# Kernel tuning notes

Measured on AMD Instinct MI355X. Metric: run time of the kernel, lower is better.

## Reference

```python
import jax, jax.numpy as jnp
import numpy as np

B, S, D = 16, 4096, 1024
DIM_K, DIM_V, NUM_HEAD = 1024, 1024, 16


def setup_inputs() -> dict:
    key = jax.random.key(0)
    ks = jax.random.split(key, 7)
    s_in = 1.0 / np.sqrt(D)
    return {
        "x": jax.random.normal(ks[0], (B, S, D), dtype=jnp.float32),
        "Wq": jax.random.normal(ks[1], (D, DIM_K), dtype=jnp.float32) * s_in,
        "bq": jnp.zeros((DIM_K,), dtype=jnp.float32),
        "Wk": jax.random.normal(ks[2], (D, DIM_K), dtype=jnp.float32) * s_in,
        "bk": jnp.zeros((DIM_K,), dtype=jnp.float32),
        "Wv": jax.random.normal(ks[3], (D, DIM_V), dtype=jnp.float32) * s_in,
        "bv": jnp.zeros((DIM_V,), dtype=jnp.float32),
    }


def reference(x, Wq, bq, Wk, bk, Wv, bv):
    H = NUM_HEAD
    b, s, _ = x.shape
    Q = x @ Wq + bq                      # (B,S,dim_k)
    K = x @ Wk + bk                      # (B,S,dim_k)
    V = x @ Wv + bv                      # (B,S,dim_v)
    Q_ = Q.reshape(b, s, H, DIM_K // H)  # (B,S,H,dk)
    K_ = K.reshape(b, s, H, DIM_K // H)
    V_ = V.reshape(b, s, H, DIM_V // H)
    # NOTE: faithful to the source quirk — scores are across HEADS (H x H)
    # at each (batch, seq) position; no 1/sqrt(dim_k) scaling (unused in source).
    scores = jnp.einsum("bshd,bsgd->bshg", Q_, K_)   # (B,S,H,H)
    atten = jax.nn.softmax(scores, axis=-1)
    out = jnp.einsum("bshg,bsgd->bshd", atten, V_)    # (B,S,H,dv_head)
    return out.reshape(b, s, -1)                      # (B,S,dim_v)
```

## Files before the change

### kernel.cpp

```cpp
#include <hip/hip_runtime.h>
#include <stdint.h>

#define M_TOTAL 65536
#define DIM     1024
#define NQKV    3072
#define NHEAD   16
#define HDIM    64

typedef __attribute__((ext_vector_type(8))) _Float16 f16x8;
typedef __attribute__((ext_vector_type(4))) _Float16 f16x4;
typedef __attribute__((ext_vector_type(4))) float    f32x4;

__global__ __launch_bounds__(256) void cvt_x_kernel(const float* __restrict__ x,
                                                    _Float16* __restrict__ xh,
                                                    int n4) {
    int i = blockIdx.x * blockDim.x + threadIdx.x;
    int stride = gridDim.x * blockDim.x;
    const float4* x4 = (const float4*)x;
    f16x4* o4 = (f16x4*)xh;
    for (; i < n4; i += stride) {
        float4 v = x4[i];
        f16x4 o;
        o[0] = (_Float16)v.x; o[1] = (_Float16)v.y;
        o[2] = (_Float16)v.z; o[3] = (_Float16)v.w;
        o4[i] = o;
    }
}

__global__ void cvt_w_kernel(const float* __restrict__ Wq,
                             const float* __restrict__ Wk,
                             const float* __restrict__ Wv,
                             _Float16* __restrict__ Wt) {
    __shared__ float tile[32][33];
    int which = blockIdx.z;
    const float* W = (which == 0) ? Wq : (which == 1) ? Wk : Wv;
    int d0 = blockIdx.y * 32, n0 = blockIdx.x * 32;
    int tx = threadIdx.x, ty = threadIdx.y;
    tile[ty][tx] = W[(size_t)(d0 + ty) * DIM + n0 + tx];
    __syncthreads();
    Wt[(size_t)(which * DIM + n0 + ty) * DIM + d0 + tx] = (_Float16)tile[tx][ty];
}

__global__ __launch_bounds__(256) void bias_kernel(const float* __restrict__ bq,
                                                   const float* __restrict__ bk,
                                                   const float* __restrict__ bv,
                                                   float* __restrict__ bias) {
    int i = blockIdx.x * 256 + threadIdx.x;
    if (i < NQKV)
        bias[i] = (i < 1024) ? bq[i] : (i < 2048) ? bk[i - 1024] : bv[i - 2048];
}


#define LDSA(slot)  ((slot) << 15)
#define LDSB(slot)  (65536 + ((slot) << 15))

#define MFMA_Q(MIBASE, NIBASE)                                                  \
    __builtin_amdgcn_s_setprio(1);                                              \
    _Pragma("unroll") for (int mi = 0; mi < 4; ++mi)                            \
    _Pragma("unroll") for (int ni = 0; ni < 2; ++ni)                            \
    _Pragma("unroll") for (int ks = 0; ks < 2; ++ks)                            \
        acc[(MIBASE) + mi][(NIBASE) + ni] = __builtin_amdgcn_mfma_f32_16x16x32_f16( \
            a[mi][ks], b[(NIBASE) + ni][ks], acc[(MIBASE) + mi][(NIBASE) + ni], 0, 0, 0); \
    __builtin_amdgcn_s_setprio(0);

__global__ __launch_bounds__(512, 2) void qkv_gemm_kernel(const _Float16* __restrict__ Xh,
                                                          const _Float16* __restrict__ Wth,
                                                          const float* __restrict__ bias,
                                                          _Float16* __restrict__ Ch) {
    extern __shared__ char smem[];

    const int bid = blockIdx.x;
    const int swz = (bid & 7) * (3072 / 8) + (bid >> 3);
    const int tm  = swz / (NQKV / 256);
    const int tn  = swz % (NQKV / 256);
    const int brow = tm * 256;
    const int bcol = tn * 256;

    const int tid = threadIdx.x;
    const int w   = tid >> 6;
    const int l   = tid & 63;
    const int wm  = w >> 2;
    const int wn  = w & 3;

    const int lrow8 = l >> 3;
    const int lcol8 = (l & 7) ^ lrow8;
    const _Float16* pAsrc = Xh  + (size_t)(brow + w * 8 + lrow8) * DIM + lcol8 * 8;
    const _Float16* pBsrc = Wth + (size_t)(bcol + w * 8 + lrow8) * DIM + lcol8 * 8;

    auto stA = [&](int slot, int kt, int half) {
        const _Float16* s = pAsrc + ((size_t)half << 17) + ((size_t)kt << 6);
        char* d = smem + LDSA(slot) + (half << 14) + (w << 10);
        __builtin_amdgcn_global_load_lds((const __attribute__((address_space(1))) void*)s,
                                         (__attribute__((address_space(3))) void*)d, 16, 0, 0);
        __builtin_amdgcn_global_load_lds((const __attribute__((address_space(1))) void*)(s + (1 << 16)),
                                         (__attribute__((address_space(3))) void*)(d + 8192), 16, 0, 0);
    };
    auto stB = [&](int slot, int kt, int half) {
        const _Float16* s = pBsrc + ((size_t)half << 17) + ((size_t)kt << 6);
        char* d = smem + LDSB(slot) + (half << 14) + (w << 10);
        __builtin_amdgcn_global_load_lds((const __attribute__((address_space(1))) void*)s,
                                         (__attribute__((address_space(3))) void*)d, 16, 0, 0);
        __builtin_amdgcn_global_load_lds((const __attribute__((address_space(1))) void*)(s + (1 << 16)),
                                         (__attribute__((address_space(3))) void*)(d + 8192), 16, 0, 0);
    };

    const int aRowB = ((wm << 7) + (l & 15)) << 7;
    const int bRowB = 65536 + (((wn << 6) + (l & 15)) << 7);
    const int xk0 = (((l >> 4) ^ (l & 7)) << 4);
    const int xk1 = ((((l >> 4) + 4) ^ (l & 7)) << 4);
    auto LDA = [&](int slot, int mi, int ks) -> f16x8 {
        return *(const f16x8*)(smem + (slot << 15) + aRowB + (mi << 11) + (ks ? xk1 : xk0));
    };
    auto LDB = [&](int slot, int ni, int ks) -> f16x8 {
        return *(const f16x8*)(smem + (slot << 15) + bRowB + (ni << 11) + (ks ? xk1 : xk0));
    };

    f32x4 acc[8][4] = {};
    f16x8 a[4][2], b[4][2];

    stB(0, 0, 0); stB(0, 0, 1);
    stA(0, 0, 0); stA(0, 0, 1);
    stB(1, 1, 0); stB(1, 1, 1);
    asm volatile("s_waitcnt vmcnt(4)" ::: "memory");
    __builtin_amdgcn_s_barrier();
    __builtin_amdgcn_sched_barrier(0);

#pragma unroll 1
    for (int i = 0; i < 7; ++i) {
        const int u = 2 * i;
#pragma unroll
        for (int mi = 0; mi < 4; ++mi) { a[mi][0] = LDA(0, mi, 0); a[mi][1] = LDA(0, mi, 1); }
#pragma unroll
        for (int ni = 0; ni < 2; ++ni) { b[ni][0] = LDB(0, ni, 0); b[ni][1] = LDB(0, ni, 1); }
        stA(1, u + 1, 0);
        __builtin_amdgcn_s_barrier();
        MFMA_Q(0, 0)
        __builtin_amdgcn_s_barrier();
        b[2][0] = LDB(0, 2, 0); b[2][1] = LDB(0, 2, 1);
        b[3][0] = LDB(0, 3, 0); b[3][1] = LDB(0, 3, 1);
        stA(1, u + 1, 1);
        __builtin_amdgcn_s_barrier();
        MFMA_Q(0, 2)
        __builtin_amdgcn_s_barrier();
#pragma unroll
        for (int mi = 0; mi < 4; ++mi) { a[mi][0] = LDA(0, mi + 4, 0); a[mi][1] = LDA(0, mi + 4, 1); }
        stB(0, u + 2, 0);
        __builtin_amdgcn_s_barrier();
        MFMA_Q(4, 0)
        __builtin_amdgcn_s_barrier();
        stB(0, u + 2, 1);
        asm volatile("s_waitcnt vmcnt(4)" ::: "memory");
        __builtin_amdgcn_s_barrier();
        __builtin_amdgcn_sched_barrier(0);
        MFMA_Q(4, 2)
        __builtin_amdgcn_s_barrier();
#pragma unroll
        for (int mi = 0; mi < 4; ++mi) { a[mi][0] = LDA(1, mi, 0); a[mi][1] = LDA(1, mi, 1); }
#pragma unroll
        for (int ni = 0; ni < 2; ++ni) { b[ni][0] = LDB(1, ni, 0); b[ni][1] = LDB(1, ni, 1); }
        stA(0, u + 2, 0);
        __builtin_amdgcn_s_barrier();
        MFMA_Q(0, 0)
        __builtin_amdgcn_s_barrier();
        b[2][0] = LDB(1, 2, 0); b[2][1] = LDB(1, 2, 1);
        b[3][0] = LDB(1, 3, 0); b[3][1] = LDB(1, 3, 1);
        stA(0, u + 2, 1);
        __builtin_amdgcn_s_barrier();
        MFMA_Q(0, 2)
        __builtin_amdgcn_s_barrier();
#pragma unroll
        for (int mi = 0; mi < 4; ++mi) { a[mi][0] = LDA(1, mi + 4, 0); a[mi][1] = LDA(1, mi + 4, 1); }
        stB(1, u + 3, 0);
        __builtin_amdgcn_s_barrier();
        MFMA_Q(4, 0)
        __builtin_amdgcn_s_barrier();
        stB(1, u + 3, 1);
        asm volatile("s_waitcnt vmcnt(4)" ::: "memory");
        __builtin_amdgcn_s_barrier();
        __builtin_amdgcn_sched_barrier(0);
        MFMA_Q(4, 2)
        __builtin_amdgcn_s_barrier();
    }

    {
#pragma unroll
        for (int mi = 0; mi < 4; ++mi) { a[mi][0] = LDA(0, mi, 0); a[mi][1] = LDA(0, mi, 1); }
#pragma unroll
        for (int ni = 0; ni < 2; ++ni) { b[ni][0] = LDB(0, ni, 0); b[ni][1] = LDB(0, ni, 1); }
        stA(1, 15, 0);
        __builtin_amdgcn_s_barrier();
        MFMA_Q(0, 0)
        __builtin_amdgcn_s_barrier();
        b[2][0] = LDB(0, 2, 0); b[2][1] = LDB(0, 2, 1);
        b[3][0] = LDB(0, 3, 0); b[3][1] = LDB(0, 3, 1);
        stA(1, 15, 1);
        __builtin_amdgcn_s_barrier();
        MFMA_Q(0, 2)
        __builtin_amdgcn_s_barrier();
#pragma unroll
        for (int mi = 0; mi < 4; ++mi) { a[mi][0] = LDA(0, mi + 4, 0); a[mi][1] = LDA(0, mi + 4, 1); }
        __builtin_amdgcn_s_barrier();
        MFMA_Q(4, 0)
        __builtin_amdgcn_s_barrier();
        asm volatile("s_waitcnt vmcnt(0)" ::: "memory");
        __builtin_amdgcn_s_barrier();
        __builtin_amdgcn_sched_barrier(0);
        MFMA_Q(4, 2)
        __builtin_amdgcn_s_barrier();
#pragma unroll
        for (int mi = 0; mi < 4; ++mi) { a[mi][0] = LDA(1, mi, 0); a[mi][1] = LDA(1, mi, 1); }
#pragma unroll
        for (int ni = 0; ni < 2; ++ni) { b[ni][0] = LDB(1, ni, 0); b[ni][1] = LDB(1, ni, 1); }
        __builtin_amdgcn_s_barrier();
        MFMA_Q(0, 0)
        __builtin_amdgcn_s_barrier();
        b[2][0] = LDB(1, 2, 0); b[2][1] = LDB(1, 2, 1);
        b[3][0] = LDB(1, 3, 0); b[3][1] = LDB(1, 3, 1);
        __builtin_amdgcn_s_barrier();
        MFMA_Q(0, 2)
        __builtin_amdgcn_s_barrier();
#pragma unroll
        for (int mi = 0; mi < 4; ++mi) { a[mi][0] = LDA(1, mi + 4, 0); a[mi][1] = LDA(1, mi + 4, 1); }
        __builtin_amdgcn_s_barrier();
        MFMA_Q(4, 0)
        MFMA_Q(4, 2)
    }

    const int r4 = (l >> 4) << 2;
#pragma unroll
    for (int ni = 0; ni < 4; ++ni) {
        const int col = bcol + (wn << 6) + (ni << 4) + (l & 15);
        const float bv = bias[col];
#pragma unroll
        for (int mi = 0; mi < 8; ++mi) {
#pragma unroll
            for (int jj = 0; jj < 4; ++jj) {
                const int row = brow + (wm << 7) + (mi << 4) + r4 + jj;
                Ch[(size_t)row * NQKV + col] = (_Float16)(acc[mi][ni][jj] + bv);
            }
        }
    }
}

__global__ __launch_bounds__(256) void attn_kernel(const _Float16* __restrict__ QKVh,
                                                   float* __restrict__ out) {
    __shared__ _Float16 vlds[4][1024];
    __shared__ float attlds[4][16][16];

    const int w = threadIdx.x >> 6, l = threadIdx.x & 63;
    const size_t p = (size_t)blockIdx.x * 4 + w;
    const _Float16* base = QKVh + p * NQKV;
    const _Float16* qrow = base;
    const _Float16* krow = base + 1024;
    const _Float16* vrow = base + 2048;
    const int h = l & 15;
    const int g4 = (l >> 4) * 4;

    *(uint4*)&vlds[w][l * 16]     = *(const uint4*)&vrow[l * 16];
    *(uint4*)&vlds[w][l * 16 + 8] = *(const uint4*)&vrow[l * 16 + 8];

    const int fo = (l & 15) * HDIM + (l >> 4) * 8;
    f16x8 aK0 = *(const f16x8*)&krow[fo];
    f16x8 aK1 = *(const f16x8*)&krow[fo + 32];
    f16x8 bQ0 = *(const f16x8*)&qrow[fo];
    f16x8 bQ1 = *(const f16x8*)&qrow[fo + 32];

    f32x4 sT = {0.f, 0.f, 0.f, 0.f};
    sT = __builtin_amdgcn_mfma_f32_16x16x32_f16(aK0, bQ0, sT, 0, 0, 0);
    sT = __builtin_amdgcn_mfma_f32_16x16x32_f16(aK1, bQ1, sT, 0, 0, 0);

    float m = fmaxf(fmaxf(sT[0], sT[1]), fmaxf(sT[2], sT[3]));
    m = fmaxf(m, __shfl_xor(m, 16));
    m = fmaxf(m, __shfl_xor(m, 32));
    float e0 = __expf(sT[0] - m), e1 = __expf(sT[1] - m);
    float e2 = __expf(sT[2] - m), e3 = __expf(sT[3] - m);
    float s = e0 + e1 + e2 + e3;
    s += __shfl_xor(s, 16);
    s += __shfl_xor(s, 32);
    const float inv = 1.0f / s;

    float4 att = make_float4(e0 * inv, e1 * inv, e2 * inv, e3 * inv);
    *(float4*)&attlds[w][h][g4] = att;
    __syncthreads();

    const int dbase = (l >> 4) * 16;
    float acc[16];
#pragma unroll
    for (int c = 0; c < 16; ++c) acc[c] = 0.f;

#pragma unroll
    for (int g = 0; g < 16; ++g) {
        const float av = attlds[w][h][g];
        f16x8 v0 = *(const f16x8*)&vlds[w][g * HDIM + dbase];
        f16x8 v1 = *(const f16x8*)&vlds[w][g * HDIM + dbase + 8];
#pragma unroll
        for (int c = 0; c < 8; ++c) {
            acc[c]     += av * (float)v0[c];
            acc[c + 8] += av * (float)v1[c];
        }
    }

    float* op = out + p * DIM + h * HDIM + dbase;
#pragma unroll
    for (int c = 0; c < 16; c += 4)
        *(float4*)(op + c) = make_float4(acc[c], acc[c + 1], acc[c + 2], acc[c + 3]);
}

extern "C" void kernel_launch(void* const* d_in, const int* in_sizes, int n_in,
                              void* d_out, int out_size, void* d_ws, size_t ws_size,
                              hipStream_t stream) {
    const float* x  = (const float*)d_in[0];
    const float* Wq = (const float*)d_in[1];
    const float* bq = (const float*)d_in[2];
    const float* Wk = (const float*)d_in[3];
    const float* bk = (const float*)d_in[4];
    const float* Wv = (const float*)d_in[5];
    const float* bv = (const float*)d_in[6];
    float* out = (float*)d_out;

    char* ws = (char*)d_ws;
    _Float16* Xh  = (_Float16*)ws;
    _Float16* Wth = (_Float16*)(ws + 134217728);
    float*    bias = (float*)(ws + 134217728 + 6291456);
    _Float16* Ch  = (_Float16*)(ws + 134217728 + 6291456 + 12288);

    static int lds_attr_set = 0;
    (void)hipFuncSetAttribute((const void*)qkv_gemm_kernel,
                              hipFuncAttributeMaxDynamicSharedMemorySize, 131072);

    hipLaunchKernelGGL(cvt_x_kernel, dim3(2048), dim3(256), 0, stream,
                       x, Xh, (M_TOTAL * DIM) / 4);
    hipLaunchKernelGGL(cvt_w_kernel, dim3(32, 32, 3), dim3(32, 32), 0, stream,
                       Wq, Wk, Wv, Wth);
    hipLaunchKernelGGL(bias_kernel, dim3(12), dim3(256), 0, stream,
                       bq, bk, bv, bias);
    hipLaunchKernelGGL(qkv_gemm_kernel, dim3((M_TOTAL / 256) * (NQKV / 256)), dim3(512), 131072, stream,
                       Xh, Wth, bias, Ch);
    hipLaunchKernelGGL(attn_kernel, dim3(M_TOTAL / 4), dim3(256), 0, stream,
                       Ch, out);
}
```

Before: 638.5 us.

## Make GEMM blocks persistent over all N tiles for each row panel

The QKV GEMM launch shrinks from one block per 256x256 output tile to one block per 256-row panel. Each block loops over all 12 column tiles as one continuous pipelined stream of K-steps, writes the epilogue and clears the accumulators between tiles. This removes per-tile pipeline prologue and drain and lets A-panel rows be reused through cache. The grid drops from 3072 to 256 blocks, which may leave CUs underused and gives up the L2-friendly tile swizzle.

New measurement: 705.8 us. 10.5% more time.

```diff
diff --git a/kernel.cpp b/kernel.cpp
--- a/kernel.cpp
+++ b/kernel.cpp
@@ -69,12 +69,8 @@
                                                           _Float16* __restrict__ Ch) {
     extern __shared__ char smem[];
 
-    const int bid = blockIdx.x;
-    const int swz = (bid & 7) * (3072 / 8) + (bid >> 3);
-    const int tm  = swz / (NQKV / 256);
-    const int tn  = swz % (NQKV / 256);
-    const int brow = tm * 256;
-    const int bcol = tn * 256;
+    const int bid  = blockIdx.x;
+    const int brow = bid * 256;
 
     const int tid = threadIdx.x;
     const int w   = tid >> 6;
@@ -85,22 +81,24 @@
     const int lrow8 = l >> 3;
     const int lcol8 = (l & 7) ^ lrow8;
     const _Float16* pAsrc = Xh  + (size_t)(brow + w * 8 + lrow8) * DIM + lcol8 * 8;
-    const _Float16* pBsrc = Wth + (size_t)(bcol + w * 8 + lrow8) * DIM + lcol8 * 8;
-
-    auto stA = [&](int slot, int kt, int half) {
-        const _Float16* s = pAsrc + ((size_t)half << 17) + ((size_t)kt << 6);
+    const _Float16* pBsrc = Wth + (size_t)(w * 8 + lrow8) * DIM + lcol8 * 8;
+
+    auto stA = [&](int slot, int s, int half) {
+        if (s > 191) s = 191;
+        const _Float16* sp = pAsrc + ((size_t)half << 17) + ((size_t)(s & 15) << 6);
         char* d = smem + LDSA(slot) + (half << 14) + (w << 10);
-        __builtin_amdgcn_global_load_lds((const __attribute__((address_space(1))) void*)s,
+        __builtin_amdgcn_global_load_lds((const __attribute__((address_space(1))) void*)sp,
                                          (__attribute__((address_space(3))) void*)d, 16, 0, 0);
-        __builtin_amdgcn_global_load_lds((const __attribute__((address_space(1))) void*)(s + (1 << 16)),
+        __builtin_amdgcn_global_load_lds((const __attribute__((address_space(1))) void*)(sp + (1 << 16)),
                                          (__attribute__((address_space(3))) void*)(d + 8192), 16, 0, 0);
     };
-    auto stB = [&](int slot, int kt, int half) {
-        const _Float16* s = pBsrc + ((size_t)half << 17) + ((size_t)kt << 6);
+    auto stB = [&](int slot, int s, int half) {
+        if (s > 191) s = 191;
+        const _Float16* sp = pBsrc + ((size_t)(s >> 4) << 18) + ((size_t)half << 17) + ((size_t)(s & 15) << 6);
         char* d = smem + LDSB(slot) + (half << 14) + (w << 10);
-        __builtin_amdgcn_global_load_lds((const __attribute__((address_space(1))) void*)s,
+        __builtin_amdgcn_global_load_lds((const __attribute__((address_space(1))) void*)sp,
                                          (__attribute__((address_space(3))) void*)d, 16, 0, 0);
-        __builtin_amdgcn_global_load_lds((const __attribute__((address_space(1))) void*)(s + (1 << 16)),
+        __builtin_amdgcn_global_load_lds((const __attribute__((address_space(1))) void*)(sp + (1 << 16)),
                                          (__attribute__((address_space(3))) void*)(d + 8192), 16, 0, 0);
     };
 
@@ -121,125 +119,94 @@
     stB(0, 0, 0); stB(0, 0, 1);
     stA(0, 0, 0); stA(0, 0, 1);
     stB(1, 1, 0); stB(1, 1, 1);
-    asm volatile("s_waitcnt vmcnt(4)" ::: "memory");
+    asm volatile("s_waitcnt vmcnt(2)" ::: "memory");
     __builtin_amdgcn_s_barrier();
     __builtin_amdgcn_sched_barrier(0);
 
 #pragma unroll 1
-    for (int i = 0; i < 7; ++i) {
-        const int u = 2 * i;
-#pragma unroll
-        for (int mi = 0; mi < 4; ++mi) { a[mi][0] = LDA(0, mi, 0); a[mi][1] = LDA(0, mi, 1); }
-#pragma unroll
-        for (int ni = 0; ni < 2; ++ni) { b[ni][0] = LDB(0, ni, 0); b[ni][1] = LDB(0, ni, 1); }
-        stA(1, u + 1, 0);
-        __builtin_amdgcn_s_barrier();
-        MFMA_Q(0, 0)
-        __builtin_amdgcn_s_barrier();
-        b[2][0] = LDB(0, 2, 0); b[2][1] = LDB(0, 2, 1);
-        b[3][0] = LDB(0, 3, 0); b[3][1] = LDB(0, 3, 1);
-        stA(1, u + 1, 1);
-        __builtin_amdgcn_s_barrier();
-        MFMA_Q(0, 2)
-        __builtin_amdgcn_s_barrier();
-#pragma unroll
-        for (int mi = 0; mi < 4; ++mi) { a[mi][0] = LDA(0, mi + 4, 0); a[mi][1] = LDA(0, mi + 4, 1); }
-        stB(0, u + 2, 0);
-        __builtin_amdgcn_s_barrier();
-        MFMA_Q(4, 0)
-        __builtin_amdgcn_s_barrier();
-        stB(0, u + 2, 1);
-        asm volatile("s_waitcnt vmcnt(4)" ::: "memory");
-        __builtin_amdgcn_s_barrier();
-        __builtin_amdgcn_sched_barrier(0);
-        MFMA_Q(4, 2)
-        __builtin_amdgcn_s_barrier();
-#pragma unroll
-        for (int mi = 0; mi < 4; ++mi) { a[mi][0] = LDA(1, mi, 0); a[mi][1] = LDA(1, mi, 1); }
-#pragma unroll
-        for (int ni = 0; ni < 2; ++ni) { b[ni][0] = LDB(1, ni, 0); b[ni][1] = LDB(1, ni, 1); }
-        stA(0, u + 2, 0);
-        __builtin_amdgcn_s_barrier();
-        MFMA_Q(0, 0)
-        __builtin_amdgcn_s_barrier();
-        b[2][0] = LDB(1, 2, 0); b[2][1] = LDB(1, 2, 1);
-        b[3][0] = LDB(1, 3, 0); b[3][1] = LDB(1, 3, 1);
-        stA(0, u + 2, 1);
-        __builtin_amdgcn_s_barrier();
-        MFMA_Q(0, 2)
-        __builtin_amdgcn_s_barrier();
-#pragma unroll
-        for (int mi = 0; mi < 4; ++mi) { a[mi][0] = LDA(1, mi + 4, 0); a[mi][1] = LDA(1, mi + 4, 1); }
-        stB(1, u + 3, 0);
-        __builtin_amdgcn_s_barrier();
-        MFMA_Q(4, 0)
-        __builtin_amdgcn_s_barrier();
-        stB(1, u + 3, 1);
-        asm volatile("s_waitcnt vmcnt(4)" ::: "memory");
-        __builtin_amdgcn_s_barrier();
-        __builtin_amdgcn_sched_barrier(0);
-        MFMA_Q(4, 2)
-        __builtin_amdgcn_s_barrier();
-    }
-
-    {
-#pragma unroll
-        for (int mi = 0; mi < 4; ++mi) { a[mi][0] = LDA(0, mi, 0); a[mi][1] = LDA(0, mi, 1); }
-#pragma unroll
-        for (int ni = 0; ni < 2; ++ni) { b[ni][0] = LDB(0, ni, 0); b[ni][1] = LDB(0, ni, 1); }
-        stA(1, 15, 0);
-        __builtin_amdgcn_s_barrier();
-        MFMA_Q(0, 0)
-        __builtin_amdgcn_s_barrier();
-        b[2][0] = LDB(0, 2, 0); b[2][1] = LDB(0, 2, 1);
-        b[3][0] = LDB(0, 3, 0); b[3][1] = LDB(0, 3, 1);
-        stA(1, 15, 1);
-        __builtin_amdgcn_s_barrier();
-        MFMA_Q(0, 2)
-        __builtin_amdgcn_s_barrier();
-#pragma unroll
-        for (int mi = 0; mi < 4; ++mi) { a[mi][0] = LDA(0, mi + 4, 0); a[mi][1] = LDA(0, mi + 4, 1); }
-        __builtin_amdgcn_s_barrier();
-        MFMA_Q(4, 0)
-        __builtin_amdgcn_s_barrier();
-        asm volatile("s_waitcnt vmcnt(0)" ::: "memory");
-        __builtin_amdgcn_s_barrier();
-        __builtin_amdgcn_sched_barrier(0);
-        MFMA_Q(4, 2)
-        __builtin_amdgcn_s_barrier();
-#pragma unroll
-        for (int mi = 0; mi < 4; ++mi) { a[mi][0] = LDA(1, mi, 0); a[mi][1] = LDA(1, mi, 1); }
-#pragma unroll
-        for (int ni = 0; ni < 2; ++ni) { b[ni][0] = LDB(1, ni, 0); b[ni][1] = LDB(1, ni, 1); }
-        __builtin_amdgcn_s_barrier();
-        MFMA_Q(0, 0)
-        __builtin_amdgcn_s_barrier();
-        b[2][0] = LDB(1, 2, 0); b[2][1] = LDB(1, 2, 1);
-        b[3][0] = LDB(1, 3, 0); b[3][1] = LDB(1, 3, 1);
-        __builtin_amdgcn_s_barrier();
-        MFMA_Q(0, 2)
-        __builtin_amdgcn_s_barrier();
-#pragma unroll
-        for (int mi = 0; mi < 4; ++mi) { a[mi][0] = LDA(1, mi + 4, 0); a[mi][1] = LDA(1, mi + 4, 1); }
-        __builtin_amdgcn_s_barrier();
-        MFMA_Q(4, 0)
-        MFMA_Q(4, 2)
-    }
-
-    const int r4 = (l >> 4) << 2;
-#pragma unroll
-    for (int ni = 0; ni < 4; ++ni) {
-        const int col = bcol + (wn << 6) + (ni << 4) + (l & 15);
-        const float bv = bias[col];
-#pragma unroll
-        for (int mi = 0; mi < 8; ++mi) {
-#pragma unroll
-            for (int jj = 0; jj < 4; ++jj) {
-                const int row = brow + (wm << 7) + (mi << 4) + r4 + jj;
-                Ch[(size_t)row * NQKV + col] = (_Float16)(acc[mi][ni][jj] + bv);
+    for (int t = 0; t < 12; ++t) {
+#pragma unroll 1
+        for (int ii = 0; ii < 8; ++ii) {
+            const int u = (t << 4) + (ii << 1);
+#pragma unroll
+            for (int mi = 0; mi < 4; ++mi) { a[mi][0] = LDA(0, mi, 0); a[mi][1] = LDA(0, mi, 1); }
+#pragma unroll
+            for (int ni = 0; ni < 2; ++ni) { b[ni][0] = LDB(0, ni, 0); b[ni][1] = LDB(0, ni, 1); }
+            stA(1, u + 1, 0);
+            __builtin_amdgcn_s_barrier();
+            MFMA_Q(0, 0)
+            __builtin_amdgcn_s_barrier();
+            b[2][0] = LDB(0, 2, 0); b[2][1] = LDB(0, 2, 1);
+            b[3][0] = LDB(0, 3, 0); b[3][1] = LDB(0, 3, 1);
+            stA(1, u + 1, 1);
+            __builtin_amdgcn_s_barrier();
+            MFMA_Q(0, 2)
+            __builtin_amdgcn_s_barrier();
+#pragma unroll
+            for (int mi = 0; mi < 4; ++mi) { a[mi][0] = LDA(0, mi + 4, 0); a[mi][1] = LDA(0, mi + 4, 1); }
+            stB(0, u + 2, 0);
+            __builtin_amdgcn_s_barrier();
+            MFMA_Q(4, 0)
+            __builtin_amdgcn_s_barrier();
+            stB(0, u + 2, 1);
+            asm volatile("s_waitcnt vmcnt(4)" ::: "memory");
+            __builtin_amdgcn_s_barrier();
+            __builtin_amdgcn_sched_barrier(0);
+            MFMA_Q(4, 2)
+            __builtin_amdgcn_s_barrier();
+#pragma unroll
+            for (int mi = 0; mi < 4; ++mi) { a[mi][0] = LDA(1, mi, 0); a[mi][1] = LDA(1, mi, 1); }
+#pragma unroll
+            for (int ni = 0; ni < 2; ++ni) { b[ni][0] = LDB(1, ni, 0); b[ni][1] = LDB(1, ni, 1); }
+            stA(0, u + 2, 0);
+            __builtin_amdgcn_s_barrier();
+            MFMA_Q(0, 0)
+            __builtin_amdgcn_s_barrier();
+            b[2][0] = LDB(1, 2, 0); b[2][1] = LDB(1, 2, 1);
+            b[3][0] = LDB(1, 3, 0); b[3][1] = LDB(1, 3, 1);
+            stA(0, u + 2, 1);
+            __builtin_amdgcn_s_barrier();
+            MFMA_Q(0, 2)
+            __builtin_amdgcn_s_barrier();
+#pragma unroll
+            for (int mi = 0; mi < 4; ++mi) { a[mi][0] = LDA(1, mi + 4, 0); a[mi][1] = LDA(1, mi + 4, 1); }
+            stB(1, u + 3, 0);
+            __builtin_amdgcn_s_barrier();
+            MFMA_Q(4, 0)
+            __builtin_amdgcn_s_barrier();
+            stB(1, u + 3, 1);
+            asm volatile("s_waitcnt vmcnt(4)" ::: "memory");
+            __builtin_amdgcn_s_barrier();
+            __builtin_amdgcn_sched_barrier(0);
+            MFMA_Q(4, 2)
+            __builtin_amdgcn_s_barrier();
+        }
+
+        {
+            const int bcol = t << 8;
+            const int r4 = (l >> 4) << 2;
+#pragma unroll
+            for (int ni = 0; ni < 4; ++ni) {
+                const int col = bcol + (wn << 6) + (ni << 4) + (l & 15);
+                const float bv = bias[col];
+#pragma unroll
+                for (int mi = 0; mi < 8; ++mi) {
+#pragma unroll
+                    for (int jj = 0; jj < 4; ++jj) {
+                        const int row = brow + (wm << 7) + (mi << 4) + r4 + jj;
+                        Ch[(size_t)row * NQKV + col] = (_Float16)(acc[mi][ni][jj] + bv);
+                    }
+                }
             }
+#pragma unroll
+            for (int mi = 0; mi < 8; ++mi)
+#pragma unroll
+                for (int ni = 0; ni < 4; ++ni)
+                    acc[mi][ni] = (f32x4){0.f, 0.f, 0.f, 0.f};
         }
     }
+
+    asm volatile("s_waitcnt vmcnt(0)" ::: "memory");
 }
 
 __global__ __launch_bounds__(256) void attn_kernel(const _Float16* __restrict__ QKVh,
@@ -324,7 +291,6 @@
     float*    bias = (float*)(ws + 134217728 + 6291456);
     _Float16* Ch  = (_Float16*)(ws + 134217728 + 6291456 + 12288);
 
-    static int lds_attr_set = 0;
     (void)hipFuncSetAttribute((const void*)qkv_gemm_kernel,
                               hipFuncAttributeMaxDynamicSharedMemorySize, 131072);
 
@@ -334,7 +300,7 @@
                        Wq, Wk, Wv, Wth);
     hipLaunchKernelGGL(bias_kernel, dim3(12), dim3(256), 0, stream,
                        bq, bk, bv, bias);
-    hipLaunchKernelGGL(qkv_gemm_kernel, dim3((M_TOTAL / 256) * (NQKV / 256)), dim3(512), 131072, stream,
+    hipLaunchKernelGGL(qkv_gemm_kernel, dim3(M_TOTAL / 256), dim3(512), 131072, stream,
                        Xh, Wth, bias, Ch);
     hipLaunchKernelGGL(attn_kernel, dim3(M_TOTAL / 4), dim3(256), 0, stream,
                        Ch, out);
```
